# Optimization experiments

Hardware: AMD Instinct MI355X
Metric: run time of the kernel (lower is better)

## Reference

```python
import jax, jax.numpy as jnp
import numpy as np

D = 768      # input_dim
O = 768      # output_dim
E = 8        # num_experts
H = 10 * D   # expert hidden dim (fixed by module: input_dim * 10)
N = 4096     # tokens


def setup_inputs() -> dict:
    key = jax.random.key(0)
    ks = jax.random.split(key, 7)
    s = lambda fan_in: 1.0 / np.sqrt(fan_in)
    x  = jax.random.normal(ks[0], (N, D), dtype=jnp.float32)
    Wg = jax.random.uniform(ks[1], (D, E), jnp.float32, -s(D), s(D))
    bg = jax.random.uniform(ks[2], (E,),   jnp.float32, -s(D), s(D))
    W1 = jax.random.uniform(ks[3], (E, D, H), jnp.float32, -s(D), s(D))
    b1 = jax.random.uniform(ks[4], (E, H),    jnp.float32, -s(D), s(D))
    W2 = jax.random.uniform(ks[5], (E, H, O), jnp.float32, -s(H), s(H))
    b2 = jax.random.uniform(ks[6], (E, O),    jnp.float32, -s(H), s(H))
    return {"x": x, "Wg": Wg, "bg": bg, "W1": W1, "b1": b1, "W2": W2, "b2": b2}


def reference(x, Wg, bg, W1, b1, W2, b2):
    # gating: softmax over experts, keep only top-1 prob (rest zeroed)
    gate_probs = jax.nn.softmax(x @ Wg + bg, axis=1)          # [N, E]
    top_vals, top_idx = jax.lax.top_k(gate_probs, 1)           # [N, 1]
    gate_masked = jnp.zeros_like(gate_probs).at[
        jnp.arange(x.shape[0]), top_idx[:, 0]].set(top_vals[:, 0])
    # dense all-experts MLP (module computes every expert for every token)
    h = jax.nn.relu(jnp.einsum('nd,edh->neh', x, W1) + b1)     # [N, E, H]
    expert_out = jnp.einsum('neh,eho->neo', h, W2) + b2        # [N, E, O]
    # bmm combine: [N,1,E] @ [N,E,O] -> [N,O]
    return jnp.einsum('ne,neo->no', gate_masked, expert_out)
```

## Files before the change

kernel.cpp:

```cpp
#include <hip/hip_runtime.h>
#include <hip/hip_bf16.h>
#include <stdint.h>

#define N_TOK 4096
#define DIM   768
#define NE    8
#define HDIM  7680
#define ODIM  768
#define G1GRID 2816
#define G2GRID 1344

typedef __bf16 bf16x8 __attribute__((ext_vector_type(8)));
typedef float f32x4 __attribute__((ext_vector_type(4)));

__device__ __forceinline__ unsigned short f2bf(float f) {
    union { float f; unsigned u; } v; v.f = f;
    return (unsigned short)((v.u + 0x7fffu + ((v.u >> 16) & 1u)) >> 16);
}

__device__ __forceinline__ unsigned cvt_pk_bf16(float lo, float hi) {
    unsigned r;
    asm("v_cvt_pk_bf16_f32 %0, %1, %2" : "=v"(r) : "v"(lo), "v"(hi));
    return r;
}

__device__ __forceinline__ void gload_lds16(const unsigned short* g, unsigned short* l) {
    __builtin_amdgcn_global_load_lds(
        (const __attribute__((address_space(1))) unsigned int*)g,
        (__attribute__((address_space(3))) unsigned int*)l, 16, 0, 0);
}

__global__ void moe_gating(const float* __restrict__ x, const float* __restrict__ Wg,
                           const float* __restrict__ bg, int* __restrict__ cnt,
                           int* __restrict__ top_e, int* __restrict__ rnk,
                           float* __restrict__ top_p) {
    const int wid  = threadIdx.x >> 6;
    const int lane = threadIdx.x & 63;
    const int t = blockIdx.x * 4 + wid;
    double p[NE];
#pragma unroll
    for (int j = 0; j < NE; ++j) p[j] = 0.0;
    const float* xr  = x  + (size_t)t * DIM + lane * 12;
    const float* wr0 = Wg + lane * 12 * NE;
#pragma unroll
    for (int i = 0; i < 12; ++i) {
        double xv = (double)xr[i];
#pragma unroll
        for (int j = 0; j < NE; ++j) p[j] += xv * (double)wr0[i * NE + j];
    }
#pragma unroll
    for (int off = 32; off >= 1; off >>= 1)
#pragma unroll
        for (int j = 0; j < NE; ++j) p[j] += __shfl_xor(p[j], off, 64);
    if (lane == 0) {
        double l[NE];
#pragma unroll
        for (int j = 0; j < NE; ++j) l[j] = p[j] + (double)bg[j];
        int be = 0; double bl = l[0];
#pragma unroll
        for (int j = 1; j < NE; ++j) if (l[j] > bl) { bl = l[j]; be = j; }
        double s = 0.0;
#pragma unroll
        for (int j = 0; j < NE; ++j) s += exp(l[j] - bl);
        int rk = atomicAdd(&cnt[be], 1);
        top_e[t] = be; rnk[t] = rk; top_p[t] = (float)(1.0 / s);
    }
}

__global__ void moe_init(int* cnt) { if (threadIdx.x < NE) cnt[threadIdx.x] = 0; }

__global__ void moe_scan(const int* __restrict__ cnt, int* __restrict__ offs,
                         int* __restrict__ mc, int* __restrict__ g1s,
                         int* __restrict__ g2s) {
    __shared__ int smc[NE];
    int tid = threadIdx.x;
    if (tid == 0) { int s = 0; for (int e = 0; e < NE; ++e) { offs[e] = s; s += cnt[e]; } }
    if (tid < NE) { smc[tid] = (cnt[tid] + 127) >> 7; mc[tid] = smc[tid]; }
    __syncthreads();
    if (tid < 8) {
        int s = 0;
        for (int j = 0; j < 60; ++j) { int p = tid + 8 * j; g1s[p] = s; s += smc[p / 60]; }
        int s2 = 0;
        for (int j = 0; j < 6; ++j)  { int p = tid + 8 * j; g2s[p] = s2; s2 += 4 * smc[p / 6]; }
    }
}

__global__ void moe_fill(const int* __restrict__ mc, const int* __restrict__ g1s,
                         const int* __restrict__ g2s, int* __restrict__ tbl1,
                         int* __restrict__ tbl2) {
    int gid = blockIdx.x * 256 + threadIdx.x;
    if (gid < G1GRID) {
        int c = gid & 7, slot = gid >> 3;
        int sel = c;
        for (int j = 0; j < 60; ++j) { int p = c + 8 * j; if (g1s[p] <= slot) sel = p; else break; }
        int e = sel / 60, n0 = sel % 60;
        int mt = slot - g1s[sel];
        tbl1[gid] = (mt < mc[e]) ? ((e << 14) | (mt << 8) | (n0 << 2)) : -1;
    } else if (gid < G1GRID + G2GRID) {
        int gg = gid - G1GRID;
        int c = gg & 7, slot = gg >> 3;
        int sel = c;
        for (int j = 0; j < 6; ++j) { int p = c + 8 * j; if (g2s[p] <= slot) sel = p; else break; }
        int e = sel / 6, n0 = sel % 6;
        int mem = slot - g2s[sel];
        int mcE = mc[e];
        int ks = mem / mcE, mt = mem - ks * mcE;
        tbl2[gg] = (mem < 4 * mcE) ? ((e << 14) | (mt << 8) | (n0 << 2) | ks) : -1;
    }
}

__global__ void moe_mkperm(const int* __restrict__ top_e, const int* __restrict__ rnk,
                           const float* __restrict__ top_p, const int* __restrict__ offs,
                           int* __restrict__ perm, float* __restrict__ gate_s) {
    int t = blockIdx.x * 256 + threadIdx.x;
    int e = top_e[t];
    int slot = offs[e] + rnk[t];
    perm[slot] = t;
    gate_s[slot] = top_p[t];
}

__global__ void moe_gather(const float* __restrict__ x, const int* __restrict__ perm,
                           unsigned short* __restrict__ Xg) {
    int slot = blockIdx.x;
    int t = perm[slot];
    const float* src = x + (size_t)t * DIM;
    unsigned short* dst = Xg + (size_t)slot * DIM;
    for (int i = threadIdx.x; i < DIM; i += 256) dst[i] = f2bf(src[i]);
}

__global__ void moe_initout(const int* __restrict__ top_e, const float* __restrict__ top_p,
                            const float* __restrict__ b2, float* __restrict__ out) {
    int t = blockIdx.x;
    int e = top_e[t];
    float gv = top_p[t];
    const float* b = b2 + (size_t)e * ODIM;
    float* o = out + (size_t)t * ODIM;
    for (int i = threadIdx.x; i < ODIM; i += 256) o[i] = gv * b[i];
}

template<int LAYER>
__global__ __launch_bounds__(256, 3) void moe_gemm(
    const unsigned short* __restrict__ A, const float* __restrict__ B,
    const float* __restrict__ bias, const int* __restrict__ cnt,
    const int* __restrict__ offs, const int* __restrict__ perm,
    const float* __restrict__ gate_s, const int* __restrict__ tbl,
    unsigned short* __restrict__ H, float* __restrict__ out) {

    constexpr int NT    = (LAYER == 1) ? HDIM : ODIM;
    constexpr int AST   = (LAYER == 1) ? DIM  : HDIM;
    constexpr int KFULL = (LAYER == 1) ? DIM  : HDIM;
    constexpr int KBLK  = (LAYER == 1) ? DIM  : HDIM / 4;
    constexpr int NITER = KBLK / 32;

    const int code = tbl[blockIdx.x];
    if (code < 0) return;
    const int e  = code >> 14;
    const int mt = (code >> 8) & 63;
    const int n0 = ((code >> 2) & 63) * 128;
    const int ks = code & 3;
    const int ne = cnt[e];
    const int base = offs[e];
    const int mlim = ne - mt * 128;
    const int kbase = ks * KBLK;

    __shared__ __align__(16) unsigned short As[3][4096];
    __shared__ __align__(16) unsigned short Bs[2][4096];

    const int tid = threadIdx.x;
    const int lane = tid & 63, w = tid >> 6;
    const int wr = w >> 1, wc = w & 1;
    const int g = lane >> 4, r = lane & 15;

    const int rl0 = 2 * w * 16 + r;
    const int rl1 = rl0 + 16;
    const int cr0 = rl0 < mlim ? rl0 : mlim - 1;
    const int cr1 = rl1 < mlim ? rl1 : mlim - 1;
    const unsigned short* aS0 = A + (size_t)(base + mt * 128 + cr0) * AST + kbase + g * 8;
    const unsigned short* aS1 = A + (size_t)(base + mt * 128 + cr1) * AST + kbase + g * 8;
    const int aD0 = (2 * w) * 512;
    const int aD1 = aD0 + 512;

    const int bn = tid & 127;
    const int kh = tid >> 7;
    const float* bS = B + (size_t)e * KFULL * NT + (size_t)(kbase + kh * 16) * NT + n0 + bn;
    const int bD = (bn >> 4) * 512 + (kh * 2) * 128 + (bn & 15) * 8;

    f32x4 acc[4][4] = {};
    float bvA[16], bvB[16];

    unsigned short* A0 = &As[0][0];
    unsigned short* A1 = &As[1][0];
    unsigned short* A2 = &As[2][0];

#define LOADB(dst_, t_)                                                        \
    do { const float* bp_ = bS + (size_t)((t_) * 32) * NT;                     \
        _Pragma("unroll")                                                      \
        for (int i_ = 0; i_ < 16; ++i_) dst_[i_] = bp_[(size_t)i_ * NT];       \
    } while (0)

#define DMA_A(t_, abase_)                                                      \
    do { gload_lds16(aS0 + (t_) * 32, (abase_) + aD0);                         \
         gload_lds16(aS1 + (t_) * 32, (abase_) + aD1); } while (0)

#define COMMITB(src_, buf_)                                                    \
    do { uint4 q0_, q1_;                                                       \
        q0_.x = cvt_pk_bf16(src_[0],  src_[1]);  q0_.y = cvt_pk_bf16(src_[2],  src_[3]);  \
        q0_.z = cvt_pk_bf16(src_[4],  src_[5]);  q0_.w = cvt_pk_bf16(src_[6],  src_[7]);  \
        q1_.x = cvt_pk_bf16(src_[8],  src_[9]);  q1_.y = cvt_pk_bf16(src_[10], src_[11]); \
        q1_.z = cvt_pk_bf16(src_[12], src_[13]); q1_.w = cvt_pk_bf16(src_[14], src_[15]); \
        *(uint4*)&Bs[buf_][bD]       = q0_;                                    \
        *(uint4*)&Bs[buf_][bD + 128] = q1_;                                    \
    } while (0)

#define PHASE_END                                                              \
    do { asm volatile("s_waitcnt lgkmcnt(0)" ::: "memory");                    \
         __builtin_amdgcn_s_barrier();                                         \
         __builtin_amdgcn_sched_barrier(0); } while (0)

#define BODY(t_, cur_, ARD_, ADMA_, LDst_, CMsrc_, MODE_)                      \
    do {                                                                       \
        bf16x8 af_[4], bf_[4];                                                 \
        _Pragma("unroll")                                                      \
        for (int m_ = 0; m_ < 4; ++m_)                                         \
            af_[m_] = *(const bf16x8*)((ARD_) + (wr * 4 + m_) * 512 + lane * 8); \
        _Pragma("unroll")                                                      \
        for (int n_ = 0; n_ < 4; ++n_)                                         \
            bf_[n_] = *(const bf16x8*)&Bs[cur_][(wc * 4 + n_) * 512 + lane * 8]; \
        if (MODE_ == 2) DMA_A((t_) + 2, ADMA_);                                \
        if (MODE_ == 2) LOADB(LDst_, (t_) + 2);                                \
        _Pragma("unroll")                                                      \
        for (int n_ = 0; n_ < 4; ++n_)                                         \
            _Pragma("unroll")                                                  \
            for (int m_ = 0; m_ < 4; ++m_)                                     \
                acc[m_][n_] = __builtin_amdgcn_mfma_f32_16x16x32_bf16(         \
                    af_[m_], bf_[n_], acc[m_][n_], 0, 0, 0);                   \
        if (MODE_ >= 1) { COMMITB(CMsrc_, (cur_) ^ 1); PHASE_END; }            \
    } while (0)

    DMA_A(0, A0);
    LOADB(bvA, 0);
    DMA_A(1, A1);
    LOADB(bvB, 1);
    COMMITB(bvA, 0);
    PHASE_END;

#pragma unroll 1
    for (int t = 0; t + 4 <= NITER; t += 2) {
        BODY(t,     0, A0, A2, bvA, bvB, 2);
        BODY(t + 1, 1, A1, A0, bvB, bvA, 2);
        unsigned short* tr_ = A2; A2 = A1; A1 = A0; A0 = tr_;
    }
    BODY(NITER - 2, 0, A0, A2, bvA, bvB, 1);
    BODY(NITER - 1, 1, A1, A2, bvB, bvA, 0);

#undef BODY
#undef PHASE_END
#undef COMMITB
#undef DMA_A
#undef LOADB

#pragma unroll
    for (int m = 0; m < 4; ++m) {
#pragma unroll
        for (int j = 0; j < 4; ++j) {
            int lrow = mt * 128 + wr * 64 + m * 16 + g * 4 + j;
            if (lrow < ne) {
                int slot = base + lrow;
#pragma unroll
                for (int n = 0; n < 4; ++n) {
                    int col = n0 + wc * 64 + n * 16 + r;
                    if constexpr (LAYER == 1) {
                        float v = acc[m][n][j] + bias[(size_t)e * NT + col];
                        v = fmaxf(v, 0.0f);
                        H[(size_t)slot * HDIM + col] = f2bf(v);
                    } else {
                        atomicAdd(&out[(size_t)perm[slot] * ODIM + col],
                                  gate_s[slot] * acc[m][n][j]);
                    }
                }
            }
        }
    }
}

extern "C" void kernel_launch(void* const* d_in, const int* in_sizes, int n_in,
                              void* d_out, int out_size, void* d_ws, size_t ws_size,
                              hipStream_t stream) {
    const float* x  = (const float*)d_in[0];
    const float* Wg = (const float*)d_in[1];
    const float* bg = (const float*)d_in[2];
    const float* W1 = (const float*)d_in[3];
    const float* b1 = (const float*)d_in[4];
    const float* W2 = (const float*)d_in[5];
    const float* b2 = (const float*)d_in[6];
    float* out = (float*)d_out;

    char* ws = (char*)d_ws;
    int*   cnt    = (int*)(ws + 0);
    int*   offs   = (int*)(ws + 64);
    int*   mc     = (int*)(ws + 128);
    int*   g1s    = (int*)(ws + 256);
    int*   g2s    = (int*)(ws + 2304);
    int*   tbl1   = (int*)(ws + 3072);
    int*   tbl2   = (int*)(ws + 14336);
    int*   top_e  = (int*)(ws + 19712);
    int*   rnk    = (int*)(ws + 19712 + 16384);
    float* top_p  = (float*)(ws + 19712 + 2 * 16384);
    int*   perm   = (int*)(ws + 19712 + 3 * 16384);
    float* gate_s = (float*)(ws + 19712 + 4 * 16384);
    unsigned short* Xg = (unsigned short*)(ws + 101632);
    unsigned short* H  = (unsigned short*)(ws + 101632 + (size_t)N_TOK * DIM * 2);

    moe_init<<<1, 64, 0, stream>>>(cnt);
    moe_gating<<<N_TOK / 4, 256, 0, stream>>>(x, Wg, bg, cnt, top_e, rnk, top_p);
    moe_scan<<<1, 64, 0, stream>>>(cnt, offs, mc, g1s, g2s);
    moe_fill<<<(G1GRID + G2GRID + 255) / 256, 256, 0, stream>>>(mc, g1s, g2s, tbl1, tbl2);
    moe_mkperm<<<N_TOK / 256, 256, 0, stream>>>(top_e, rnk, top_p, offs, perm, gate_s);
    moe_gather<<<N_TOK, 256, 0, stream>>>(x, perm, Xg);
    moe_initout<<<N_TOK, 256, 0, stream>>>(top_e, top_p, b2, out);

    moe_gemm<1><<<G1GRID, 256, 0, stream>>>(Xg, W1, b1, cnt, offs, perm, gate_s, tbl1, H, out);
    moe_gemm<2><<<G2GRID, 256, 0, stream>>>(H, W2, b2, cnt, offs, perm, gate_s, tbl2, H, out);
}
```

Measured before the change: 369.0 us.

## Replace split-K atomics with partial buffers and reduce; stage epilogue through LDS

Measured after the change: 364.0 us. No clear change (-1.4%).

```diff
diff --git a/kernel.cpp b/kernel.cpp
--- a/kernel.cpp
+++ b/kernel.cpp
@@ -128,23 +128,28 @@
     for (int i = threadIdx.x; i < DIM; i += 256) dst[i] = f2bf(src[i]);
 }
 
-__global__ void moe_initout(const int* __restrict__ top_e, const float* __restrict__ top_p,
-                            const float* __restrict__ b2, float* __restrict__ out) {
-    int t = blockIdx.x;
+__global__ void moe_reduce(const float* __restrict__ part, const int* __restrict__ perm,
+                           const float* __restrict__ gate_s, const int* __restrict__ top_e,
+                           const float* __restrict__ b2, float* __restrict__ out) {
+    int slot = blockIdx.x;
+    int t = perm[slot];
     int e = top_e[t];
-    float gv = top_p[t];
-    const float* b = b2 + (size_t)e * ODIM;
-    float* o = out + (size_t)t * ODIM;
-    for (int i = threadIdx.x; i < ODIM; i += 256) o[i] = gv * b[i];
+    float gv = gate_s[slot];
+    int c = threadIdx.x * 4;
+    f32x4 s = *(const f32x4*)&b2[(size_t)e * ODIM + c];
+#pragma unroll
+    for (int ks = 0; ks < 4; ++ks)
+        s += *(const f32x4*)&part[((size_t)ks * N_TOK + slot) * ODIM + c];
+    s *= gv;
+    *(f32x4*)&out[(size_t)t * ODIM + c] = s;
 }
 
 template<int LAYER>
 __global__ __launch_bounds__(256, 3) void moe_gemm(
     const unsigned short* __restrict__ A, const float* __restrict__ B,
     const float* __restrict__ bias, const int* __restrict__ cnt,
-    const int* __restrict__ offs, const int* __restrict__ perm,
-    const float* __restrict__ gate_s, const int* __restrict__ tbl,
-    unsigned short* __restrict__ H, float* __restrict__ out) {
+    const int* __restrict__ offs, const int* __restrict__ tbl,
+    unsigned short* __restrict__ H, float* __restrict__ part) {
 
     constexpr int NT    = (LAYER == 1) ? HDIM : ODIM;
     constexpr int AST   = (LAYER == 1) ? DIM  : HDIM;
@@ -163,8 +168,7 @@
     const int mlim = ne - mt * 128;
     const int kbase = ks * KBLK;
 
-    __shared__ __align__(16) unsigned short As[3][4096];
-    __shared__ __align__(16) unsigned short Bs[2][4096];
+    __shared__ __align__(16) unsigned short LDSu[5][4096];
 
     const int tid = threadIdx.x;
     const int lane = tid & 63, w = tid >> 6;
@@ -188,9 +192,10 @@
     f32x4 acc[4][4] = {};
     float bvA[16], bvB[16];
 
-    unsigned short* A0 = &As[0][0];
-    unsigned short* A1 = &As[1][0];
-    unsigned short* A2 = &As[2][0];
+    unsigned short* A0 = &LDSu[0][0];
+    unsigned short* A1 = &LDSu[1][0];
+    unsigned short* A2 = &LDSu[2][0];
+    unsigned short* Bsb = &LDSu[3][0];
 
 #define LOADB(dst_, t_)                                                        \
     do { const float* bp_ = bS + (size_t)((t_) * 32) * NT;                     \
@@ -208,8 +213,8 @@
         q0_.z = cvt_pk_bf16(src_[4],  src_[5]);  q0_.w = cvt_pk_bf16(src_[6],  src_[7]);  \
         q1_.x = cvt_pk_bf16(src_[8],  src_[9]);  q1_.y = cvt_pk_bf16(src_[10], src_[11]); \
         q1_.z = cvt_pk_bf16(src_[12], src_[13]); q1_.w = cvt_pk_bf16(src_[14], src_[15]); \
-        *(uint4*)&Bs[buf_][bD]       = q0_;                                    \
-        *(uint4*)&Bs[buf_][bD + 128] = q1_;                                    \
+        *(uint4*)(Bsb + (buf_) * 4096 + bD)       = q0_;                       \
+        *(uint4*)(Bsb + (buf_) * 4096 + bD + 128) = q1_;                       \
     } while (0)
 
 #define PHASE_END                                                              \
@@ -225,7 +230,8 @@
             af_[m_] = *(const bf16x8*)((ARD_) + (wr * 4 + m_) * 512 + lane * 8); \
         _Pragma("unroll")                                                      \
         for (int n_ = 0; n_ < 4; ++n_)                                         \
-            bf_[n_] = *(const bf16x8*)&Bs[cur_][(wc * 4 + n_) * 512 + lane * 8]; \
+            bf_[n_] = *(const bf16x8*)(Bsb + (cur_) * 4096 +                   \
+                                       (wc * 4 + n_) * 512 + lane * 8);        \
         if (MODE_ == 2) DMA_A((t_) + 2, ADMA_);                                \
         if (MODE_ == 2) LOADB(LDst_, (t_) + 2);                                \
         _Pragma("unroll")                                                      \
@@ -259,26 +265,63 @@
 #undef DMA_A
 #undef LOADB
 
-#pragma unroll
-    for (int m = 0; m < 4; ++m) {
-#pragma unroll
-        for (int j = 0; j < 4; ++j) {
-            int lrow = mt * 128 + wr * 64 + m * 16 + g * 4 + j;
-            if (lrow < ne) {
-                int slot = base + lrow;
-#pragma unroll
-                for (int n = 0; n < 4; ++n) {
-                    int col = n0 + wc * 64 + n * 16 + r;
-                    if constexpr (LAYER == 1) {
-                        float v = acc[m][n][j] + bias[(size_t)e * NT + col];
-                        v = fmaxf(v, 0.0f);
-                        H[(size_t)slot * HDIM + col] = f2bf(v);
-                    } else {
-                        atomicAdd(&out[(size_t)perm[slot] * ODIM + col],
-                                  gate_s[slot] * acc[m][n][j]);
+    __builtin_amdgcn_s_barrier();
+    unsigned short* cw = &LDSu[0][0] + w * 5120;
+
+    if constexpr (LAYER == 1) {
+        float bfv[4];
+#pragma unroll
+        for (int n = 0; n < 4; ++n)
+            bfv[n] = bias[(size_t)e * NT + n0 + wc * 64 + n * 16 + r];
+#pragma unroll
+        for (int m = 0; m < 4; ++m)
+#pragma unroll
+            for (int n = 0; n < 4; ++n)
+#pragma unroll
+                for (int j = 0; j < 4; ++j) {
+                    int rowl = m * 16 + g * 4 + j;
+                    int coll = n * 16 + r;
+                    float v = fmaxf(acc[m][n][j] + bfv[n], 0.0f);
+                    cw[rowl * 64 + (coll ^ ((rowl & 7) << 3))] = f2bf(v);
+                }
+        asm volatile("s_waitcnt lgkmcnt(0)" ::: "memory");
+#pragma unroll
+        for (int i = 0; i < 8; ++i) {
+            int rowl = i * 8 + (lane >> 3);
+            int ch = ((lane & 7) ^ (rowl & 7)) * 8;
+            uint4 q = *(const uint4*)&cw[rowl * 64 + ch];
+            int gcol = ((lane & 7) * 8);
+            int lrow = mt * 128 + wr * 64 + rowl;
+            if (lrow < ne)
+                *(uint4*)&H[(size_t)(base + lrow) * HDIM + n0 + wc * 64 + gcol] = q;
+        }
+    } else {
+        float* cwf = (float*)cw;
+#pragma unroll
+        for (int h = 0; h < 2; ++h) {
+#pragma unroll
+            for (int mm = 0; mm < 2; ++mm)
+#pragma unroll
+                for (int n = 0; n < 4; ++n)
+#pragma unroll
+                    for (int j = 0; j < 4; ++j) {
+                        int rowl = mm * 16 + g * 4 + j;
+                        int coll = n * 16 + r;
+                        cwf[rowl * 64 + (coll ^ ((rowl & 7) << 2))] = acc[h * 2 + mm][n][j];
                     }
-                }
+            asm volatile("s_waitcnt lgkmcnt(0)" ::: "memory");
+#pragma unroll
+            for (int i = 0; i < 8; ++i) {
+                int rowl = (i >> 1) * 8 + (lane >> 3);
+                int ci = (i & 1) * 8 + (lane & 7);
+                int cs = ((i & 1) * 8 + ((lane & 7) ^ (rowl & 7))) * 4;
+                f32x4 q = *(const f32x4*)&cwf[rowl * 64 + cs];
+                int lrow = mt * 128 + wr * 64 + h * 32 + rowl;
+                if (lrow < ne)
+                    *(f32x4*)&part[((size_t)ks * N_TOK + (base + lrow)) * ODIM
+                                   + n0 + wc * 64 + ci * 4] = q;
             }
+            asm volatile("s_waitcnt lgkmcnt(0)" ::: "memory");
         }
     }
 }
@@ -308,8 +351,9 @@
     float* top_p  = (float*)(ws + 19712 + 2 * 16384);
     int*   perm   = (int*)(ws + 19712 + 3 * 16384);
     float* gate_s = (float*)(ws + 19712 + 4 * 16384);
-    unsigned short* Xg = (unsigned short*)(ws + 101632);
-    unsigned short* H  = (unsigned short*)(ws + 101632 + (size_t)N_TOK * DIM * 2);
+    unsigned short* Xg   = (unsigned short*)(ws + 101632);
+    unsigned short* H    = (unsigned short*)(ws + 101632 + (size_t)N_TOK * DIM * 2);
+    float*          part = (float*)(ws + 69307648ull);
 
     moe_init<<<1, 64, 0, stream>>>(cnt);
     moe_gating<<<N_TOK / 4, 256, 0, stream>>>(x, Wg, bg, cnt, top_e, rnk, top_p);
@@ -317,8 +361,8 @@
     moe_fill<<<(G1GRID + G2GRID + 255) / 256, 256, 0, stream>>>(mc, g1s, g2s, tbl1, tbl2);
     moe_mkperm<<<N_TOK / 256, 256, 0, stream>>>(top_e, rnk, top_p, offs, perm, gate_s);
     moe_gather<<<N_TOK, 256, 0, stream>>>(x, perm, Xg);
-    moe_initout<<<N_TOK, 256, 0, stream>>>(top_e, top_p, b2, out);
-
-    moe_gemm<1><<<G1GRID, 256, 0, stream>>>(Xg, W1, b1, cnt, offs, perm, gate_s, tbl1, H, out);
-    moe_gemm<2><<<G2GRID, 256, 0, stream>>>(H, W2, b2, cnt, offs, perm, gate_s, tbl2, H, out);
-}
+
+    moe_gemm<1><<<G1GRID, 256, 0, stream>>>(Xg, W1, b1, cnt, offs, tbl1, H, part);
+    moe_gemm<2><<<G2GRID, 256, 0, stream>>>(H, W2, b2, cnt, offs, tbl2, H, part);
+    moe_reduce<<<N_TOK, 192, 0, stream>>>(part, perm, gate_s, top_e, b2, out);
+}
```

## Use 8 waves per GEMM block with 2x4 warp grid

Applied to the files above, without the earlier changes.

Measured after the change: 388.2 us. 5.2% more time.

```diff
diff --git a/kernel.cpp b/kernel.cpp
--- a/kernel.cpp
+++ b/kernel.cpp
@@ -139,7 +139,7 @@
 }
 
 template<int LAYER>
-__global__ __launch_bounds__(256, 3) void moe_gemm(
+__global__ __launch_bounds__(512, 2) void moe_gemm(
     const unsigned short* __restrict__ A, const float* __restrict__ B,
     const float* __restrict__ bias, const int* __restrict__ cnt,
     const int* __restrict__ offs, const int* __restrict__ perm,
@@ -168,25 +168,21 @@
 
     const int tid = threadIdx.x;
     const int lane = tid & 63, w = tid >> 6;
-    const int wr = w >> 1, wc = w & 1;
+    const int wr = w >> 2, wc = w & 3;
     const int g = lane >> 4, r = lane & 15;
 
-    const int rl0 = 2 * w * 16 + r;
-    const int rl1 = rl0 + 16;
-    const int cr0 = rl0 < mlim ? rl0 : mlim - 1;
-    const int cr1 = rl1 < mlim ? rl1 : mlim - 1;
-    const unsigned short* aS0 = A + (size_t)(base + mt * 128 + cr0) * AST + kbase + g * 8;
-    const unsigned short* aS1 = A + (size_t)(base + mt * 128 + cr1) * AST + kbase + g * 8;
-    const int aD0 = (2 * w) * 512;
-    const int aD1 = aD0 + 512;
+    const int rl = w * 16 + r;
+    const int cr = rl < mlim ? rl : mlim - 1;
+    const unsigned short* aS = A + (size_t)(base + mt * 128 + cr) * AST + kbase + g * 8;
+    const int aD = w * 512;
 
     const int bn = tid & 127;
     const int kh = tid >> 7;
-    const float* bS = B + (size_t)e * KFULL * NT + (size_t)(kbase + kh * 16) * NT + n0 + bn;
-    const int bD = (bn >> 4) * 512 + (kh * 2) * 128 + (bn & 15) * 8;
-
-    f32x4 acc[4][4] = {};
-    float bvA[16], bvB[16];
+    const float* bS = B + (size_t)e * KFULL * NT + (size_t)(kbase + kh * 8) * NT + n0 + bn;
+    const int bD = (bn >> 4) * 512 + kh * 128 + (bn & 15) * 8;
+
+    f32x4 acc[4][2] = {};
+    float bvA[8], bvB[8];
 
     unsigned short* A0 = &As[0][0];
     unsigned short* A1 = &As[1][0];
@@ -195,21 +191,19 @@
 #define LOADB(dst_, t_)                                                        \
     do { const float* bp_ = bS + (size_t)((t_) * 32) * NT;                     \
         _Pragma("unroll")                                                      \
-        for (int i_ = 0; i_ < 16; ++i_) dst_[i_] = bp_[(size_t)i_ * NT];       \
+        for (int i_ = 0; i_ < 8; ++i_) dst_[i_] = bp_[(size_t)i_ * NT];        \
     } while (0)
 
 #define DMA_A(t_, abase_)                                                      \
-    do { gload_lds16(aS0 + (t_) * 32, (abase_) + aD0);                         \
-         gload_lds16(aS1 + (t_) * 32, (abase_) + aD1); } while (0)
+    do { gload_lds16(aS + (t_) * 32, (abase_) + aD); } while (0)
 
 #define COMMITB(src_, buf_)                                                    \
-    do { uint4 q0_, q1_;                                                       \
-        q0_.x = cvt_pk_bf16(src_[0],  src_[1]);  q0_.y = cvt_pk_bf16(src_[2],  src_[3]);  \
-        q0_.z = cvt_pk_bf16(src_[4],  src_[5]);  q0_.w = cvt_pk_bf16(src_[6],  src_[7]);  \
-        q1_.x = cvt_pk_bf16(src_[8],  src_[9]);  q1_.y = cvt_pk_bf16(src_[10], src_[11]); \
-        q1_.z = cvt_pk_bf16(src_[12], src_[13]); q1_.w = cvt_pk_bf16(src_[14], src_[15]); \
-        *(uint4*)&Bs[buf_][bD]       = q0_;                                    \
-        *(uint4*)&Bs[buf_][bD + 128] = q1_;                                    \
+    do { uint4 q_;                                                             \
+        q_.x = cvt_pk_bf16(src_[0], src_[1]);                                  \
+        q_.y = cvt_pk_bf16(src_[2], src_[3]);                                  \
+        q_.z = cvt_pk_bf16(src_[4], src_[5]);                                  \
+        q_.w = cvt_pk_bf16(src_[6], src_[7]);                                  \
+        *(uint4*)&Bs[buf_][bD] = q_;                                           \
     } while (0)
 
 #define PHASE_END                                                              \
@@ -219,17 +213,17 @@
 
 #define BODY(t_, cur_, ARD_, ADMA_, LDst_, CMsrc_, MODE_)                      \
     do {                                                                       \
-        bf16x8 af_[4], bf_[4];                                                 \
+        bf16x8 af_[4], bf_[2];                                                 \
         _Pragma("unroll")                                                      \
         for (int m_ = 0; m_ < 4; ++m_)                                         \
             af_[m_] = *(const bf16x8*)((ARD_) + (wr * 4 + m_) * 512 + lane * 8); \
         _Pragma("unroll")                                                      \
-        for (int n_ = 0; n_ < 4; ++n_)                                         \
-            bf_[n_] = *(const bf16x8*)&Bs[cur_][(wc * 4 + n_) * 512 + lane * 8]; \
+        for (int n_ = 0; n_ < 2; ++n_)                                         \
+            bf_[n_] = *(const bf16x8*)&Bs[cur_][(wc * 2 + n_) * 512 + lane * 8]; \
         if (MODE_ == 2) DMA_A((t_) + 2, ADMA_);                                \
         if (MODE_ == 2) LOADB(LDst_, (t_) + 2);                                \
         _Pragma("unroll")                                                      \
-        for (int n_ = 0; n_ < 4; ++n_)                                         \
+        for (int n_ = 0; n_ < 2; ++n_)                                         \
             _Pragma("unroll")                                                  \
             for (int m_ = 0; m_ < 4; ++m_)                                     \
                 acc[m_][n_] = __builtin_amdgcn_mfma_f32_16x16x32_bf16(         \
@@ -267,8 +261,8 @@
             if (lrow < ne) {
                 int slot = base + lrow;
 #pragma unroll
-                for (int n = 0; n < 4; ++n) {
-                    int col = n0 + wc * 64 + n * 16 + r;
+                for (int n = 0; n < 2; ++n) {
+                    int col = n0 + wc * 32 + n * 16 + r;
                     if constexpr (LAYER == 1) {
                         float v = acc[m][n][j] + bias[(size_t)e * NT + col];
                         v = fmaxf(v, 0.0f);
@@ -319,6 +313,6 @@
     moe_gather<<<N_TOK, 256, 0, stream>>>(x, perm, Xg);
     moe_initout<<<N_TOK, 256, 0, stream>>>(top_e, top_p, b2, out);
 
-    moe_gemm<1><<<G1GRID, 256, 0, stream>>>(Xg, W1, b1, cnt, offs, perm, gate_s, tbl1, H, out);
-    moe_gemm<2><<<G2GRID, 256, 0, stream>>>(H, W2, b2, cnt, offs, perm, gate_s, tbl2, H, out);
-}
+    moe_gemm<1><<<G1GRID, 512, 0, stream>>>(Xg, W1, b1, cnt, offs, perm, gate_s, tbl1, H, out);
+    moe_gemm<2><<<G2GRID, 512, 0, stream>>>(H, W2, b2, cnt, offs, perm, gate_s, tbl2, H, out);
+}
```

## Make MoE GEMMs persistent and prefetch next tile during epilogue

Applied to the files above, without the earlier changes.

Result: no change. 372.7 us (+1.0%).

```diff
diff --git a/kernel.cpp b/kernel.cpp
--- a/kernel.cpp
+++ b/kernel.cpp
@@ -7,8 +7,9 @@
 #define NE    8
 #define HDIM  7680
 #define ODIM  768
-#define G1GRID 2816
-#define G2GRID 1344
+#define PGRID   768
+#define TBL1LEN 3072
+#define TBL2LEN 1536
 
 typedef __bf16 bf16x8 __attribute__((ext_vector_type(8)));
 typedef float f32x4 __attribute__((ext_vector_type(4)));
@@ -89,15 +90,15 @@
                          const int* __restrict__ g2s, int* __restrict__ tbl1,
                          int* __restrict__ tbl2) {
     int gid = blockIdx.x * 256 + threadIdx.x;
-    if (gid < G1GRID) {
+    if (gid < TBL1LEN) {
         int c = gid & 7, slot = gid >> 3;
         int sel = c;
         for (int j = 0; j < 60; ++j) { int p = c + 8 * j; if (g1s[p] <= slot) sel = p; else break; }
         int e = sel / 60, n0 = sel % 60;
         int mt = slot - g1s[sel];
         tbl1[gid] = (mt < mc[e]) ? ((e << 14) | (mt << 8) | (n0 << 2)) : -1;
-    } else if (gid < G1GRID + G2GRID) {
-        int gg = gid - G1GRID;
+    } else if (gid < TBL1LEN + TBL2LEN) {
+        int gg = gid - TBL1LEN;
         int c = gg & 7, slot = gg >> 3;
         int sel = c;
         for (int j = 0; j < 6; ++j) { int p = c + 8 * j; if (g2s[p] <= slot) sel = p; else break; }
@@ -151,17 +152,7 @@
     constexpr int KFULL = (LAYER == 1) ? DIM  : HDIM;
     constexpr int KBLK  = (LAYER == 1) ? DIM  : HDIM / 4;
     constexpr int NITER = KBLK / 32;
-
-    const int code = tbl[blockIdx.x];
-    if (code < 0) return;
-    const int e  = code >> 14;
-    const int mt = (code >> 8) & 63;
-    const int n0 = ((code >> 2) & 63) * 128;
-    const int ks = code & 3;
-    const int ne = cnt[e];
-    const int base = offs[e];
-    const int mlim = ne - mt * 128;
-    const int kbase = ks * KBLK;
+    constexpr int TBLEN = (LAYER == 1) ? TBL1LEN : TBL2LEN;
 
     __shared__ __align__(16) unsigned short As[3][4096];
     __shared__ __align__(16) unsigned short Bs[2][4096];
@@ -170,24 +161,36 @@
     const int lane = tid & 63, w = tid >> 6;
     const int wr = w >> 1, wc = w & 1;
     const int g = lane >> 4, r = lane & 15;
-
-    const int rl0 = 2 * w * 16 + r;
-    const int rl1 = rl0 + 16;
-    const int cr0 = rl0 < mlim ? rl0 : mlim - 1;
-    const int cr1 = rl1 < mlim ? rl1 : mlim - 1;
-    const unsigned short* aS0 = A + (size_t)(base + mt * 128 + cr0) * AST + kbase + g * 8;
-    const unsigned short* aS1 = A + (size_t)(base + mt * 128 + cr1) * AST + kbase + g * 8;
     const int aD0 = (2 * w) * 512;
     const int aD1 = aD0 + 512;
-
-    const int bn = tid & 127;
+    const int bnn = tid & 127;
     const int kh = tid >> 7;
-    const float* bS = B + (size_t)e * KFULL * NT + (size_t)(kbase + kh * 16) * NT + n0 + bn;
-    const int bD = (bn >> 4) * 512 + (kh * 2) * 128 + (bn & 15) * 8;
-
-    f32x4 acc[4][4] = {};
+    const int bD = (bnn >> 4) * 512 + (kh * 2) * 128 + (bnn & 15) * 8;
+
+    int idx = blockIdx.x;
+    int code = tbl[idx];
+    if (code < 0) return;
+
+    int ce, cmt, cn0, cks, cne, cbase;
+    const unsigned short *aS0, *aS1;
+    const float* bS;
+
+#define DECODE_SET(cd_)                                                        \
+    do { ce = (cd_) >> 14; cmt = ((cd_) >> 8) & 63;                            \
+         cn0 = (((cd_) >> 2) & 63) * 128; cks = (cd_) & 3;                     \
+         cne = cnt[ce]; cbase = offs[ce];                                      \
+         int mlim_ = cne - cmt * 128;                                          \
+         int kb_ = cks * KBLK;                                                 \
+         int rl0_ = 2 * w * 16 + r, rl1_ = rl0_ + 16;                          \
+         int cr0_ = rl0_ < mlim_ ? rl0_ : mlim_ - 1;                           \
+         int cr1_ = rl1_ < mlim_ ? rl1_ : mlim_ - 1;                           \
+         aS0 = A + (size_t)(cbase + cmt * 128 + cr0_) * AST + kb_ + g * 8;     \
+         aS1 = A + (size_t)(cbase + cmt * 128 + cr1_) * AST + kb_ + g * 8;     \
+         bS  = B + (size_t)ce * KFULL * NT + (size_t)(kb_ + kh * 16) * NT      \
+               + cn0 + bnn;                                                    \
+    } while (0)
+
     float bvA[16], bvB[16];
-
     unsigned short* A0 = &As[0][0];
     unsigned short* A1 = &As[1][0];
     unsigned short* A2 = &As[2][0];
@@ -237,50 +240,76 @@
         if (MODE_ >= 1) { COMMITB(CMsrc_, (cur_) ^ 1); PHASE_END; }            \
     } while (0)
 
+    DECODE_SET(code);
     DMA_A(0, A0);
     LOADB(bvA, 0);
     DMA_A(1, A1);
     LOADB(bvB, 1);
-    COMMITB(bvA, 0);
-    PHASE_END;
+
+    while (true) {
+        COMMITB(bvA, 0);
+        PHASE_END;
+        f32x4 acc[4][4] = {};
 
 #pragma unroll 1
-    for (int t = 0; t + 4 <= NITER; t += 2) {
-        BODY(t,     0, A0, A2, bvA, bvB, 2);
-        BODY(t + 1, 1, A1, A0, bvB, bvA, 2);
-        unsigned short* tr_ = A2; A2 = A1; A1 = A0; A0 = tr_;
-    }
-    BODY(NITER - 2, 0, A0, A2, bvA, bvB, 1);
-    BODY(NITER - 1, 1, A1, A2, bvB, bvA, 0);
+        for (int t = 0; t + 4 <= NITER; t += 2) {
+            BODY(t,     0, A0, A2, bvA, bvB, 2);
+            BODY(t + 1, 1, A1, A0, bvB, bvA, 2);
+            unsigned short* tr_ = A2; A2 = A1; A1 = A0; A0 = tr_;
+        }
+        BODY(NITER - 2, 0, A0, A2, bvA, bvB, 1);
+        BODY(NITER - 1, 1, A1, A2, bvB, bvA, 0);
+
+        const int oe = ce, omt = cmt, on0 = cn0, oks = cks, one_ = cne, obase = cbase;
+        (void)oks;
+
+        idx += PGRID;
+        bool have_next = false;
+        if (idx < TBLEN) {
+            int ncode = tbl[idx];
+            if (ncode >= 0) {
+                have_next = true;
+                DECODE_SET(ncode);
+                unsigned short* tr_ = A1; A1 = A2; A2 = tr_;
+                DMA_A(0, A0);
+                LOADB(bvA, 0);
+                DMA_A(1, A1);
+                LOADB(bvB, 1);
+            }
+        }
+
+#pragma unroll
+        for (int m = 0; m < 4; ++m) {
+#pragma unroll
+            for (int j = 0; j < 4; ++j) {
+                int lrow = omt * 128 + wr * 64 + m * 16 + g * 4 + j;
+                if (lrow < one_) {
+                    int slot = obase + lrow;
+#pragma unroll
+                    for (int n = 0; n < 4; ++n) {
+                        int col = on0 + wc * 64 + n * 16 + r;
+                        if constexpr (LAYER == 1) {
+                            float v = acc[m][n][j] + bias[(size_t)oe * NT + col];
+                            v = fmaxf(v, 0.0f);
+                            H[(size_t)slot * HDIM + col] = f2bf(v);
+                        } else {
+                            atomicAdd(&out[(size_t)perm[slot] * ODIM + col],
+                                      gate_s[slot] * acc[m][n][j]);
+                        }
+                    }
+                }
+            }
+        }
+
+        if (!have_next) return;
+    }
 
 #undef BODY
 #undef PHASE_END
 #undef COMMITB
 #undef DMA_A
 #undef LOADB
-
-#pragma unroll
-    for (int m = 0; m < 4; ++m) {
-#pragma unroll
-        for (int j = 0; j < 4; ++j) {
-            int lrow = mt * 128 + wr * 64 + m * 16 + g * 4 + j;
-            if (lrow < ne) {
-                int slot = base + lrow;
-#pragma unroll
-                for (int n = 0; n < 4; ++n) {
-                    int col = n0 + wc * 64 + n * 16 + r;
-                    if constexpr (LAYER == 1) {
-                        float v = acc[m][n][j] + bias[(size_t)e * NT + col];
-                        v = fmaxf(v, 0.0f);
-                        H[(size_t)slot * HDIM + col] = f2bf(v);
-                    } else {
-                        atomicAdd(&out[(size_t)perm[slot] * ODIM + col],
-                                  gate_s[slot] * acc[m][n][j]);
-                    }
-                }
-            }
-        }
-    }
+#undef DECODE_SET
 }
 
 extern "C" void kernel_launch(void* const* d_in, const int* in_sizes, int n_in,
@@ -302,23 +331,23 @@
     int*   g1s    = (int*)(ws + 256);
     int*   g2s    = (int*)(ws + 2304);
     int*   tbl1   = (int*)(ws + 3072);
-    int*   tbl2   = (int*)(ws + 14336);
-    int*   top_e  = (int*)(ws + 19712);
-    int*   rnk    = (int*)(ws + 19712 + 16384);
-    float* top_p  = (float*)(ws + 19712 + 2 * 16384);
-    int*   perm   = (int*)(ws + 19712 + 3 * 16384);
-    float* gate_s = (float*)(ws + 19712 + 4 * 16384);
-    unsigned short* Xg = (unsigned short*)(ws + 101632);
-    unsigned short* H  = (unsigned short*)(ws + 101632 + (size_t)N_TOK * DIM * 2);
+    int*   tbl2   = (int*)(ws + 15360);
+    int*   top_e  = (int*)(ws + 24576);
+    int*   rnk    = (int*)(ws + 24576 + 16384);
+    float* top_p  = (float*)(ws + 24576 + 2 * 16384);
+    int*   perm   = (int*)(ws + 24576 + 3 * 16384);
+    float* gate_s = (float*)(ws + 24576 + 4 * 16384);
+    unsigned short* Xg = (unsigned short*)(ws + 106496);
+    unsigned short* H  = (unsigned short*)(ws + 106496 + (size_t)N_TOK * DIM * 2);
 
     moe_init<<<1, 64, 0, stream>>>(cnt);
     moe_gating<<<N_TOK / 4, 256, 0, stream>>>(x, Wg, bg, cnt, top_e, rnk, top_p);
     moe_scan<<<1, 64, 0, stream>>>(cnt, offs, mc, g1s, g2s);
-    moe_fill<<<(G1GRID + G2GRID + 255) / 256, 256, 0, stream>>>(mc, g1s, g2s, tbl1, tbl2);
+    moe_fill<<<(TBL1LEN + TBL2LEN) / 256, 256, 0, stream>>>(mc, g1s, g2s, tbl1, tbl2);
     moe_mkperm<<<N_TOK / 256, 256, 0, stream>>>(top_e, rnk, top_p, offs, perm, gate_s);
     moe_gather<<<N_TOK, 256, 0, stream>>>(x, perm, Xg);
     moe_initout<<<N_TOK, 256, 0, stream>>>(top_e, top_p, b2, out);
 
-    moe_gemm<1><<<G1GRID, 256, 0, stream>>>(Xg, W1, b1, cnt, offs, perm, gate_s, tbl1, H, out);
-    moe_gemm<2><<<G2GRID, 256, 0, stream>>>(H, W2, b2, cnt, offs, perm, gate_s, tbl2, H, out);
-}
+    moe_gemm<1><<<PGRID, 256, 0, stream>>>(Xg, W1, b1, cnt, offs, perm, gate_s, tbl1, H, out);
+    moe_gemm<2><<<PGRID, 256, 0, stream>>>(H, W2, b2, cnt, offs, perm, gate_s, tbl2, H, out);
+}
```
